# Optimization experiments

Measured on AMD Instinct MI355X. Metric: run time of the kernel, lower is better.

## Reference

```python
import jax, jax.numpy as jnp
import numpy as np

V, E, H, L, C, B, T = 50000, 1024, 512, 2, 24, 32, 512


def _lstm_layer(x, Wih, Whh, bih, bhh):
    # x: [T, B, D]; PyTorch gate order i, f, g, o stacked along 4H.
    Hh = Whh.shape[1]
    Bb = x.shape[1]
    bias = bih + bhh

    def step(carry, xt):
        h, c = carry
        g = xt @ Wih.T + h @ Whh.T + bias  # [B, 4H]
        i, f, gg, o = jnp.split(g, 4, axis=-1)
        i = jax.nn.sigmoid(i)
        f = jax.nn.sigmoid(f)
        gg = jnp.tanh(gg)
        o = jax.nn.sigmoid(o)
        c = f * c + i * gg
        h = o * jnp.tanh(c)
        return (h, c), h

    init = (jnp.zeros((Bb, Hh), x.dtype), jnp.zeros((Bb, Hh), x.dtype))
    _, hs = jax.lax.scan(step, init, x)
    return hs  # [T, B, H]


def _bilstm(x, w_ih, w_hh, b_ih, b_hh):
    # stacked weights: [L, 2(dir), 4H, D] / [L, 2, 4H, H] / [L, 2, 4H]
    out = x
    for l in range(w_ih.shape[0]):
        fwd = _lstm_layer(out, w_ih[l, 0], w_hh[l, 0], b_ih[l, 0], b_hh[l, 0])
        bwd = _lstm_layer(out[::-1], w_ih[l, 1], w_hh[l, 1], b_ih[l, 1], b_hh[l, 1])[::-1]
        out = jnp.concatenate([fwd, bwd], axis=-1)
    return out  # [T, B, 2H]


def _crf_llh(em, tags, start, end, trans):
    # em: [T, B, C], tags: [T, B]; torchcrf log-likelihood, reduction='sum', full mask.
    # numerator: score of the gold tag path
    em_sc = jnp.take_along_axis(em, tags[:, :, None], axis=2)[:, :, 0].sum(0)  # [B]
    tr_sc = trans[tags[:-1], tags[1:]].sum(0)  # [B]
    num = start[tags[0]] + em_sc + tr_sc + end[tags[-1]]

    # denominator: forward algorithm (logsumexp DP over tag dim)
    def step(alpha, em_t):
        nxt = jax.nn.logsumexp(alpha[:, :, None] + trans[None, :, :] + em_t[:, None, :], axis=1)
        return nxt, None

    alpha0 = start[None, :] + em[0]  # [B, C]
    alphaT, _ = jax.lax.scan(step, alpha0, em[1:])
    logZ = jax.nn.logsumexp(alphaT + end[None, :], axis=1)  # [B]
    return jnp.sum(num - logZ)


def setup_inputs() -> dict:
    key = jax.random.key(0)
    ks = jax.random.split(key, 12)
    k = 1.0 / np.sqrt(H)  # PyTorch LSTM/Linear init scale
    u = lambda kk, shp, s: jax.random.uniform(kk, shp, jnp.float32, -s, s)
    return {
        "x": jax.random.randint(ks[0], (B, T), 0, V),
        "labels": jax.random.randint(ks[1], (B, T), 0, C),
        "emb_table": jax.random.normal(ks[2], (V, E), jnp.float32),
        "w_ih": u(ks[3], (L, 2, 4 * H, E), k),   # E == 2H so all layers share input dim
        "w_hh": u(ks[4], (L, 2, 4 * H, H), k),
        "b_ih": u(ks[5], (L, 2, 4 * H), k),
        "b_hh": u(ks[6], (L, 2, 4 * H), k),
        "fc_w": u(ks[7], (C, 2 * H), 1.0 / np.sqrt(2 * H)),
        "fc_b": u(ks[8], (C,), 1.0 / np.sqrt(2 * H)),
        "crf_start": u(ks[9], (C,), 0.1),
        "crf_end": u(ks[10], (C,), 0.1),
        "crf_trans": u(ks[11], (C, C), 0.1),
    }


def reference(x, labels, emb_table, w_ih, w_hh, b_ih, b_hh, fc_w, fc_b, crf_start, crf_end, crf_trans):
    embed = emb_table[x]                      # [B, T, E]
    xt = jnp.transpose(embed, (1, 0, 2))      # [T, B, E]
    h = _bilstm(xt, w_ih, w_hh, b_ih, b_hh)   # [T, B, 2H] (dropout is identity in eval)
    logits = jnp.einsum('tbh,ch->tbc', h, fc_w) + fc_b  # [T, B, C]
    llh = _crf_llh(logits, jnp.transpose(labels), crf_start, crf_end, crf_trans)
    return jnp.transpose(logits, (0, 1, 2)).transpose(1, 0, 2), -llh
```

## Files before the change

### kernel.cpp

```cpp
#include <hip/hip_runtime.h>


typedef __bf16 bf16;
typedef _Float16 f16;
typedef __bf16 bf16x8 __attribute__((ext_vector_type(8)));
typedef __bf16 bf16x4 __attribute__((ext_vector_type(4)));
typedef _Float16 f16x4 __attribute__((ext_vector_type(4)));
typedef float f32x4 __attribute__((ext_vector_type(4)));
typedef unsigned int u32;
typedef unsigned long long u64;

#define TT 512
#define BB 32
#define HH 512
#define CC_ 24
#define MROWS 16384
#define KDIM 1024
#define NGATE 2048

__device__ __forceinline__ f32x4 mfma16(bf16x8 a, bf16x8 b, f32x4 c) {
  return __builtin_amdgcn_mfma_f32_16x16x32_bf16(a, b, c, 0, 0, 0);
}
__device__ __forceinline__ float sigmoidf_(float x) { return 1.f / (1.f + __expf(-x)); }
__device__ __forceinline__ float tanhf_(float x) {
  float e = __expf(2.f * x);
  return 1.f - 2.f / (e + 1.f);
}

__global__ __launch_bounds__(256) void convert_w_k(
    const float* __restrict__ wih, const float* __restrict__ whh, const float* __restrict__ fcw,
    bf16* __restrict__ wihb, bf16* __restrict__ whhb, bf16* __restrict__ fcwb) {
  const int n1 = (2 * 2 * NGATE * KDIM) / 4;
  const int n2 = (2 * 2 * NGATE * HH) / 4;
  const int n3 = (32 * KDIM) / 4;
  int stride = gridDim.x * blockDim.x;
  for (int i = blockIdx.x * blockDim.x + threadIdx.x; i < n1 + n2 + n3; i += stride) {
    float4 v;
    bf16* dst;
    if (i < n1) {
      v = ((const float4*)wih)[i];
      dst = wihb + (size_t)i * 4;
    } else if (i < n1 + n2) {
      int j = i - n1;
      v = ((const float4*)whh)[j];
      dst = whhb + (size_t)j * 4;
    } else {
      int j = i - n1 - n2;
      if ((j >> 8) < CC_) v = ((const float4*)fcw)[j];
      else                v = make_float4(0.f, 0.f, 0.f, 0.f);
      dst = fcwb + (size_t)j * 4;
    }
    bf16x4 o; o[0] = (bf16)v.x; o[1] = (bf16)v.y; o[2] = (bf16)v.z; o[3] = (bf16)v.w;
    *(bf16x4*)dst = o;
  }
}

__global__ __launch_bounds__(64) void embed_k(const int* __restrict__ x,
                                              const float* __restrict__ emb,
                                              bf16* __restrict__ xt) {
  int row = blockIdx.x;
  int t = row >> 5, b = row & 31;
  int tok = x[b * TT + t];
  const float4* src = (const float4*)(emb + (size_t)tok * KDIM);
  bf16* dst = xt + (size_t)row * KDIM;
  int i = threadIdx.x;
#pragma unroll
  for (int c = 0; c < 4; ++c) {
    float4 v = src[i + 64 * c];
    bf16x4 o; o[0] = (bf16)v.x; o[1] = (bf16)v.y; o[2] = (bf16)v.z; o[3] = (bf16)v.w;
    *(bf16x4*)(dst + (size_t)(i + 64 * c) * 4) = o;
  }
}

__global__ __launch_bounds__(256, 2) void gemm_in_k(
    const bf16* __restrict__ A, const bf16* __restrict__ W,
    const float* __restrict__ bih, const float* __restrict__ bhh,
    f16* __restrict__ Gh) {
  __shared__ bf16 As[128 * 72];
  __shared__ bf16 Ws[128 * 72];
  int dir = blockIdx.z;
  const bf16* Wd = W + (size_t)dir * NGATE * KDIM;
  const float* bi = bih + dir * NGATE;
  const float* bh = bhh + dir * NGATE;
  f16* G = Gh + (size_t)dir * 64 * MROWS * 32;
  int m0 = blockIdx.y * 128;
  int n0 = blockIdx.x * 128;
  int tid = threadIdx.x;
  int lane = tid & 63, wave = tid >> 6;
  int wm = wave >> 1, wn = wave & 1;
  int cn = lane & 15, quad = lane >> 4;

  f32x4 zz = {0.f, 0.f, 0.f, 0.f};
  f32x4 acc[4][4];
#pragma unroll
  for (int a = 0; a < 4; ++a)
#pragma unroll
    for (int b = 0; b < 4; ++b) acc[a][b] = zz;

  for (int k0 = 0; k0 < KDIM; k0 += 64) {
    __syncthreads();
#pragma unroll
    for (int j = 0; j < 4; ++j) {
      int cch = tid + 256 * j;
      int row = cch >> 3, kq = cch & 7;
      *(bf16x8*)&As[row * 72 + kq * 8] =
          *(const bf16x8*)&A[(size_t)(m0 + row) * KDIM + k0 + kq * 8];
      *(bf16x8*)&Ws[row * 72 + kq * 8] =
          *(const bf16x8*)&Wd[(size_t)(n0 + row) * KDIM + k0 + kq * 8];
    }
    __syncthreads();
#pragma unroll
    for (int kc = 0; kc < 2; ++kc) {
      bf16x8 af[4], bw[4];
#pragma unroll
      for (int mt = 0; mt < 4; ++mt)
        af[mt] = *(const bf16x8*)&As[(wm * 64 + mt * 16 + cn) * 72 + kc * 32 + quad * 8];
#pragma unroll
      for (int nt = 0; nt < 4; ++nt)
        bw[nt] = *(const bf16x8*)&Ws[(wn * 64 + nt * 16 + cn) * 72 + kc * 32 + quad * 8];
#pragma unroll
      for (int mt = 0; mt < 4; ++mt)
#pragma unroll
        for (int nt = 0; nt < 4; ++nt)
          acc[mt][nt] = mfma16(af[mt], bw[nt], acc[mt][nt]);
    }
  }
#pragma unroll
  for (int nt = 0; nt < 4; ++nt) {
    int n = n0 + wn * 64 + nt * 16 + cn;
    float bias = bi[n] + bh[n];
    int col = n & 511, gate = n >> 9;
    size_t base = (size_t)(col >> 3) * MROWS * 32 + (size_t)(col & 7) * 4 + gate;
#pragma unroll
    for (int mt = 0; mt < 4; ++mt) {
#pragma unroll
      for (int r = 0; r < 4; ++r) {
        int row = m0 + wm * 64 + mt * 16 + quad * 4 + r;
        G[base + (size_t)row * 32] = (f16)(acc[mt][nt][r] + bias);
      }
    }
  }
}

__global__ __launch_bounds__(64) void rec_k(
    const f16* __restrict__ Gin,
    const bf16* __restrict__ Whh,
    bf16* __restrict__ hbuf,
    u64* __restrict__ hx,
    u32* __restrict__ flags) {
  int wg = blockIdx.x;
  int dir = blockIdx.y;
  int lane = threadIdx.x;
  int cn = lane & 15, quad = lane >> 4;
  int j0 = wg * 8;
  const bf16* Wd = Whh + (size_t)dir * NGATE * HH;
  const f16* Gw = Gin + ((size_t)dir * 64 + wg) * MROWS * 32;
  u64* hxd = hx + (size_t)dir * TT * 4096;
  u32* fl = flags + (size_t)dir * TT * 64;

  __shared__ bf16 Bl[2 * 16 * 520];
  __shared__ bf16 hS[32][8];
  for (int c = lane; c < 2 * 16 * 64; c += 64) {
    int col = c >> 6;
    int kc8 = c & 63;
    int nt = col >> 4, ccn = col & 15;
    int gate = nt * 2 + (ccn >> 3);
    int jj_ = ccn & 7;
    int n = gate * HH + j0 + jj_;
    *(bf16x8*)&Bl[col * 520 + kc8 * 8] = *(const bf16x8*)&Wd[(size_t)n * HH + kc8 * 8];
  }
  __syncthreads();

  float cst[2][4];
#pragma unroll
  for (int mt = 0; mt < 2; ++mt)
#pragma unroll
    for (int r = 0; r < 4; ++r) cst[mt][r] = 0.f;
  bool active = cn < 8;
  int jj = cn & 7;
  f32x4 zz = {0.f, 0.f, 0.f, 0.f};

  int pb = lane >> 1, half = lane & 1;
  int sIdx = (j0 >> 5) * 256 + (((pb >= 16) ? 2 : 0) + half) * 64 +
             ((j0 >> 3) & 3) * 16 + (pb & 15);
  size_t hbOff = ((size_t)pb * KDIM + dir * HH + j0 + half * 4);

  for (int s = 0; s < TT; ++s) {
    int t = dir ? (TT - 1 - s) : s;
    f16x4 gp_[2][4];
    if (active) {
#pragma unroll
      for (int mt = 0; mt < 2; ++mt)
#pragma unroll
        for (int r = 0; r < 4; ++r) {
          int b = mt * 16 + quad * 4 + r;
          gp_[mt][r] = *(const f16x4*)&Gw[(size_t)(t * BB + b) * 32 + jj * 4];
        }
    }
    f32x4 acc[2][2];
    acc[0][0] = zz; acc[0][1] = zz; acc[1][0] = zz; acc[1][1] = zz;
    if (s > 0) {
      int tp = dir ? (t + 1) : (t - 1);
      u32* f = fl + (size_t)(s - 1) * 64;
      while (__hip_atomic_load(&f[lane], __ATOMIC_RELAXED, __HIP_MEMORY_SCOPE_AGENT) == 0u)
        __builtin_amdgcn_s_sleep(1);
      asm volatile("s_waitcnt vmcnt(0)" ::: "memory");
      const u64* hb8 = hxd + (size_t)tp * 4096;
#pragma unroll 4
      for (int kk = 0; kk < 16; ++kk) {
        union { u64 u[2]; bf16x8 v; } a0, a1;
        a0.u[0] = __hip_atomic_load(&hb8[kk * 256 + lane],       __ATOMIC_RELAXED, __HIP_MEMORY_SCOPE_AGENT);
        a0.u[1] = __hip_atomic_load(&hb8[kk * 256 + 64 + lane],  __ATOMIC_RELAXED, __HIP_MEMORY_SCOPE_AGENT);
        a1.u[0] = __hip_atomic_load(&hb8[kk * 256 + 128 + lane], __ATOMIC_RELAXED, __HIP_MEMORY_SCOPE_AGENT);
        a1.u[1] = __hip_atomic_load(&hb8[kk * 256 + 192 + lane], __ATOMIC_RELAXED, __HIP_MEMORY_SCOPE_AGENT);
        bf16x8 b0 = *(const bf16x8*)&Bl[(0 * 16 + cn) * 520 + kk * 32 + quad * 8];
        bf16x8 b1 = *(const bf16x8*)&Bl[(1 * 16 + cn) * 520 + kk * 32 + quad * 8];
        acc[0][0] = mfma16(a0.v, b0, acc[0][0]);
        acc[0][1] = mfma16(a0.v, b1, acc[0][1]);
        acc[1][0] = mfma16(a1.v, b0, acc[1][0]);
        acc[1][1] = mfma16(a1.v, b1, acc[1][1]);
      }
    }
#pragma unroll
    for (int mt = 0; mt < 2; ++mt) {
#pragma unroll
      for (int r = 0; r < 4; ++r) {
        float ip = acc[mt][0][r], gp = acc[mt][1][r];
        float fp = __shfl(ip, lane + 8);
        float op = __shfl(gp, lane + 8);
        if (active) {
          float xi = ip + (float)gp_[mt][r][0];
          float xf = fp + (float)gp_[mt][r][1];
          float xg = gp + (float)gp_[mt][r][2];
          float xo = op + (float)gp_[mt][r][3];
          float it = sigmoidf_(xi);
          float ft = sigmoidf_(xf);
          float gt = tanhf_(xg);
          float ot = sigmoidf_(xo);
          float cc = ft * cst[mt][r] + it * gt;
          cst[mt][r] = cc;
          int b = mt * 16 + quad * 4 + r;
          hS[b][jj] = (bf16)(ot * tanhf_(cc));
        }
      }
    }
    __syncthreads();
    u64 pv = *(const u64*)&hS[pb][half * 4];
    __hip_atomic_store(&hxd[(size_t)t * 4096 + sIdx], pv, __ATOMIC_RELAXED,
                       __HIP_MEMORY_SCOPE_AGENT);
    *(u64*)&hbuf[(size_t)(t * BB) * KDIM + hbOff] = pv;
    asm volatile("s_waitcnt vmcnt(0)" ::: "memory");
    if (lane == 0)
      __hip_atomic_store(&fl[(size_t)s * 64 + wg], 1u, __ATOMIC_RELAXED,
                         __HIP_MEMORY_SCOPE_AGENT);
  }
}

__global__ __launch_bounds__(64) void gemm_fc_k(
    const bf16* __restrict__ hbuf,
    const bf16* __restrict__ fcw,
    const float* __restrict__ fcb,
    float* __restrict__ outp) {
  int m0 = blockIdx.x * 16;
  int lane = threadIdx.x;
  int cn = lane & 15, quad = lane >> 4;
  f32x4 acc0 = {0.f, 0.f, 0.f, 0.f}, acc1 = {0.f, 0.f, 0.f, 0.f};
  for (int k0 = 0; k0 < KDIM; k0 += 32) {
    bf16x8 a  = *(const bf16x8*)&hbuf[(size_t)(m0 + cn) * KDIM + k0 + quad * 8];
    bf16x8 b0 = *(const bf16x8*)&fcw[(size_t)cn * KDIM + k0 + quad * 8];
    bf16x8 b1 = *(const bf16x8*)&fcw[(size_t)(cn + 16) * KDIM + k0 + quad * 8];
    acc0 = mfma16(a, b0, acc0);
    acc1 = mfma16(a, b1, acc1);
  }
#pragma unroll
  for (int r = 0; r < 4; ++r) {
    int row = m0 + quad * 4 + r;
    int t = row >> 5, b = row & 31;
    float* o = outp + (size_t)b * (TT * CC_) + (size_t)t * CC_;
    o[cn] = acc0[r] + fcb[cn];
    int c1 = cn + 16;
    if (c1 < CC_) o[c1] = acc1[r] + fcb[c1];
  }
  if (blockIdx.x == 0 && lane == 0) outp[(size_t)BB * TT * CC_] = 0.f;
}

__global__ __launch_bounds__(64) void crf_k(
    const float* __restrict__ em,
    const int* __restrict__ labels,
    const float* __restrict__ start_, const float* __restrict__ end_,
    const float* __restrict__ trans, float* __restrict__ result) {
  int b = blockIdx.x;
  int j = threadIdx.x;
  bool act = j < CC_;
  int jc = act ? j : 0;
  float tcol[CC_];
#pragma unroll
  for (int i = 0; i < CC_; ++i) tcol[i] = trans[i * CC_ + jc];
  const float* emb_ = em + (size_t)b * (TT * CC_);
  float alpha = act ? (start_[jc] + emb_[jc]) : -1e30f;
  for (int t = 1; t < TT; ++t) {
    float m = -1e30f;
#pragma unroll
    for (int i = 0; i < CC_; ++i) {
      float ai = __shfl(alpha, i);
      m = fmaxf(m, ai + tcol[i]);
    }
    float ssum = 0.f;
#pragma unroll
    for (int i = 0; i < CC_; ++i) {
      float ai = __shfl(alpha, i);
      ssum += __expf(ai + tcol[i] - m);
    }
    float na = m + __logf(ssum) + emb_[(size_t)t * CC_ + jc];
    alpha = act ? na : -1e30f;
  }
  float v = act ? (alpha + end_[jc]) : -1e30f;
  float mm = v;
#pragma unroll
  for (int off = 32; off; off >>= 1) mm = fmaxf(mm, __shfl_xor(mm, off));
  float e = act ? __expf(v - mm) : 0.f;
#pragma unroll
  for (int off = 32; off; off >>= 1) e += __shfl_xor(e, off);
  float logZ = mm + __logf(e);
  float part = 0.f;
  for (int t = j; t < TT; t += 64) {
    int tag = labels[b * TT + t];
    part += emb_[(size_t)t * CC_ + tag];
    if (t < TT - 1) part += trans[tag * CC_ + labels[b * TT + t + 1]];
  }
#pragma unroll
  for (int off = 32; off; off >>= 1) part += __shfl_xor(part, off);
  if (j == 0) {
    float num = part + start_[labels[b * TT]] + end_[labels[b * TT + TT - 1]];
    atomicAdd(result, logZ - num);
  }
}

extern "C" void kernel_launch(void* const* d_in, const int* in_sizes, int n_in,
                              void* d_out, int out_size, void* d_ws, size_t ws_size,
                              hipStream_t stream) {
  const int*   x      = (const int*)d_in[0];
  const int*   labels = (const int*)d_in[1];
  const float* emb    = (const float*)d_in[2];
  const float* w_ih   = (const float*)d_in[3];
  const float* w_hh   = (const float*)d_in[4];
  const float* b_ih   = (const float*)d_in[5];
  const float* b_hh   = (const float*)d_in[6];
  const float* fc_w   = (const float*)d_in[7];
  const float* fc_b   = (const float*)d_in[8];
  const float* crf_s  = (const float*)d_in[9];
  const float* crf_e  = (const float*)d_in[10];
  const float* crf_t  = (const float*)d_in[11];
  float* out = (float*)d_out;
  (void)in_sizes; (void)n_in; (void)out_size; (void)ws_size;

  char* ws = (char*)d_ws;
  bf16* xt    = (bf16*)ws;
  bf16* h0    = (bf16*)(ws + 33554432);
  bf16* h1    = (bf16*)(ws + 67108864);
  bf16* wihb  = (bf16*)(ws + 100663296);
  bf16* whhb  = (bf16*)(ws + 117440512);
  bf16* fcwb  = (bf16*)(ws + 125829120);
  f16*  gin   = (f16*)(ws + 125894656);
  u64*  hx    = (u64*)(ws + 260112384);
  u32*  flags = (u32*)(ws + 293666816);

  hipMemsetAsync(flags, 0, 2 * 2 * TT * 64 * sizeof(u32), stream);
  convert_w_k<<<2048, 256, 0, stream>>>(w_ih, w_hh, fc_w, wihb, whhb, fcwb);
  embed_k<<<MROWS, 64, 0, stream>>>(x, emb, xt);

  gemm_in_k<<<dim3(16, 128, 2), 256, 0, stream>>>(xt, wihb, b_ih, b_hh, gin);
  rec_k<<<dim3(64, 2), 64, 0, stream>>>(gin, whhb, h0, hx, flags);
  gemm_in_k<<<dim3(16, 128, 2), 256, 0, stream>>>(
      h0, wihb + (size_t)2 * NGATE * KDIM, b_ih + 2 * NGATE, b_hh + 2 * NGATE, gin);
  rec_k<<<dim3(64, 2), 64, 0, stream>>>(
      gin, whhb + (size_t)2 * NGATE * HH, h1, hx, flags + 2 * TT * 64);

  gemm_fc_k<<<MROWS / 16, 64, 0, stream>>>(h1, fcwb, fc_b, out);
  crf_k<<<BB, 64, 0, stream>>>(out, labels, crf_s, crf_e, crf_t,
                               out + (size_t)BB * TT * CC_);
}
```

Baseline: 9.725 ms.

## Merge both LSTM directions into one workgroup and use counter-based step sync

The recurrent kernel now has each of 64 workgroups process both the forward and backward directions, interleaved within each time step. This halves the grid and holds both directions' Whh slices in LDS. The per-workgroup flag array, which every lane polled, is replaced by one atomic counter per step that each workgroup increments and waiters poll until it reaches 64. The h exchange layout also changes so lanes read 16-byte vectors directly, and the second layer now gets separate hx and counter regions. The aim is to hide one direction's sync latency behind the other direction's work and to make polling cheaper. The cost is that the two directions are now serialized within one workgroup.

Result: slower. 13.88 ms (+42.7%).

```diff
diff --git a/kernel.cpp b/kernel.cpp
--- a/kernel.cpp
+++ b/kernel.cpp
@@ -142,117 +142,123 @@
   }
 }
 
-__global__ __launch_bounds__(64) void rec_k(
+__global__ __launch_bounds__(64) void rec2_k(
     const f16* __restrict__ Gin,
     const bf16* __restrict__ Whh,
     bf16* __restrict__ hbuf,
     u64* __restrict__ hx,
-    u32* __restrict__ flags) {
+    u32* __restrict__ cnt) {
+  __builtin_amdgcn_fence(__ATOMIC_ACQUIRE, "agent");
   int wg = blockIdx.x;
-  int dir = blockIdx.y;
   int lane = threadIdx.x;
   int cn = lane & 15, quad = lane >> 4;
   int j0 = wg * 8;
-  const bf16* Wd = Whh + (size_t)dir * NGATE * HH;
-  const f16* Gw = Gin + ((size_t)dir * 64 + wg) * MROWS * 32;
-  u64* hxd = hx + (size_t)dir * TT * 4096;
-  u32* fl = flags + (size_t)dir * TT * 64;
-
-  __shared__ bf16 Bl[2 * 16 * 520];
-  __shared__ bf16 hS[32][8];
-  for (int c = lane; c < 2 * 16 * 64; c += 64) {
-    int col = c >> 6;
-    int kc8 = c & 63;
-    int nt = col >> 4, ccn = col & 15;
-    int gate = nt * 2 + (ccn >> 3);
-    int jj_ = ccn & 7;
-    int n = gate * HH + j0 + jj_;
-    *(bf16x8*)&Bl[col * 520 + kc8 * 8] = *(const bf16x8*)&Wd[(size_t)n * HH + kc8 * 8];
+
+  __shared__ bf16 Bl[2][32 * 520];
+  __shared__ bf16 hS[2][32][8];
+
+#pragma unroll
+  for (int d = 0; d < 2; ++d) {
+    const bf16* Wd = Whh + (size_t)d * NGATE * HH;
+    for (int c = lane; c < 32 * 64; c += 64) {
+      int col = c >> 6, kc8 = c & 63;
+      int nt = col >> 4, ccn = col & 15;
+      int gate = nt * 2 + (ccn >> 3);
+      int n = gate * HH + j0 + (ccn & 7);
+      *(bf16x8*)&Bl[d][col * 520 + kc8 * 8] = *(const bf16x8*)&Wd[(size_t)n * HH + kc8 * 8];
+    }
   }
   __syncthreads();
 
-  float cst[2][4];
-#pragma unroll
-  for (int mt = 0; mt < 2; ++mt)
-#pragma unroll
-    for (int r = 0; r < 4; ++r) cst[mt][r] = 0.f;
+  float cst[2][2][4];
+#pragma unroll
+  for (int d = 0; d < 2; ++d)
+#pragma unroll
+    for (int mt = 0; mt < 2; ++mt)
+#pragma unroll
+      for (int r = 0; r < 4; ++r) cst[d][mt][r] = 0.f;
+
   bool active = cn < 8;
   int jj = cn & 7;
   f32x4 zz = {0.f, 0.f, 0.f, 0.f};
-
   int pb = lane >> 1, half = lane & 1;
-  int sIdx = (j0 >> 5) * 256 + (((pb >= 16) ? 2 : 0) + half) * 64 +
-             ((j0 >> 3) & 3) * 16 + (pb & 15);
-  size_t hbOff = ((size_t)pb * KDIM + dir * HH + j0 + half * 4);
+  const f16* Gw[2] = { Gin + (size_t)wg * MROWS * 32,
+                       Gin + (size_t)(64 + wg) * MROWS * 32 };
+  u64* hxd[2] = { hx, hx + (size_t)TT * 4096 };
 
   for (int s = 0; s < TT; ++s) {
-    int t = dir ? (TT - 1 - s) : s;
-    f16x4 gp_[2][4];
+    int tt_[2]; tt_[0] = s; tt_[1] = TT - 1 - s;
+    f16x4 gp[2][2][4];
     if (active) {
 #pragma unroll
-      for (int mt = 0; mt < 2; ++mt)
-#pragma unroll
-        for (int r = 0; r < 4; ++r) {
-          int b = mt * 16 + quad * 4 + r;
-          gp_[mt][r] = *(const f16x4*)&Gw[(size_t)(t * BB + b) * 32 + jj * 4];
-        }
-    }
-    f32x4 acc[2][2];
-    acc[0][0] = zz; acc[0][1] = zz; acc[1][0] = zz; acc[1][1] = zz;
-    if (s > 0) {
-      int tp = dir ? (t + 1) : (t - 1);
-      u32* f = fl + (size_t)(s - 1) * 64;
-      while (__hip_atomic_load(&f[lane], __ATOMIC_RELAXED, __HIP_MEMORY_SCOPE_AGENT) == 0u)
-        __builtin_amdgcn_s_sleep(1);
-      asm volatile("s_waitcnt vmcnt(0)" ::: "memory");
-      const u64* hb8 = hxd + (size_t)tp * 4096;
+      for (int d = 0; d < 2; ++d)
+#pragma unroll
+        for (int mt = 0; mt < 2; ++mt)
+#pragma unroll
+          for (int r = 0; r < 4; ++r) {
+            int b = mt * 16 + quad * 4 + r;
+            gp[d][mt][r] = *(const f16x4*)&Gw[d][(size_t)(tt_[d] * BB + b) * 32 + jj * 4];
+          }
+    }
+#pragma unroll
+    for (int d = 0; d < 2; ++d) {
+      int t = tt_[d];
+      f32x4 acc[2][2];
+      acc[0][0] = zz; acc[0][1] = zz; acc[1][0] = zz; acc[1][1] = zz;
+      if (s > 0) {
+        int tp = d ? (t + 1) : (t - 1);
+        const u32* cp = &cnt[d * TT + s - 1];
+        while (__hip_atomic_load(cp, __ATOMIC_RELAXED, __HIP_MEMORY_SCOPE_AGENT) < 64u)
+          __builtin_amdgcn_s_sleep(1);
+        asm volatile("" ::: "memory");
+        const uint4* hb16 = (const uint4*)(hxd[d] + (size_t)tp * 4096);
 #pragma unroll 4
-      for (int kk = 0; kk < 16; ++kk) {
-        union { u64 u[2]; bf16x8 v; } a0, a1;
-        a0.u[0] = __hip_atomic_load(&hb8[kk * 256 + lane],       __ATOMIC_RELAXED, __HIP_MEMORY_SCOPE_AGENT);
-        a0.u[1] = __hip_atomic_load(&hb8[kk * 256 + 64 + lane],  __ATOMIC_RELAXED, __HIP_MEMORY_SCOPE_AGENT);
-        a1.u[0] = __hip_atomic_load(&hb8[kk * 256 + 128 + lane], __ATOMIC_RELAXED, __HIP_MEMORY_SCOPE_AGENT);
-        a1.u[1] = __hip_atomic_load(&hb8[kk * 256 + 192 + lane], __ATOMIC_RELAXED, __HIP_MEMORY_SCOPE_AGENT);
-        bf16x8 b0 = *(const bf16x8*)&Bl[(0 * 16 + cn) * 520 + kk * 32 + quad * 8];
-        bf16x8 b1 = *(const bf16x8*)&Bl[(1 * 16 + cn) * 520 + kk * 32 + quad * 8];
-        acc[0][0] = mfma16(a0.v, b0, acc[0][0]);
-        acc[0][1] = mfma16(a0.v, b1, acc[0][1]);
-        acc[1][0] = mfma16(a1.v, b0, acc[1][0]);
-        acc[1][1] = mfma16(a1.v, b1, acc[1][1]);
-      }
-    }
-#pragma unroll
-    for (int mt = 0; mt < 2; ++mt) {
-#pragma unroll
-      for (int r = 0; r < 4; ++r) {
-        float ip = acc[mt][0][r], gp = acc[mt][1][r];
-        float fp = __shfl(ip, lane + 8);
-        float op = __shfl(gp, lane + 8);
-        if (active) {
-          float xi = ip + (float)gp_[mt][r][0];
-          float xf = fp + (float)gp_[mt][r][1];
-          float xg = gp + (float)gp_[mt][r][2];
-          float xo = op + (float)gp_[mt][r][3];
-          float it = sigmoidf_(xi);
-          float ft = sigmoidf_(xf);
-          float gt = tanhf_(xg);
-          float ot = sigmoidf_(xo);
-          float cc = ft * cst[mt][r] + it * gt;
-          cst[mt][r] = cc;
-          int b = mt * 16 + quad * 4 + r;
-          hS[b][jj] = (bf16)(ot * tanhf_(cc));
+        for (int kk = 0; kk < 16; ++kk) {
+          int kc = kk * 4 + quad;
+          union { uint4 u; bf16x8 v; } a0, a1;
+          a0.u = hb16[kc * 32 + cn];
+          a1.u = hb16[kc * 32 + cn + 16];
+          bf16x8 b0 = *(const bf16x8*)&Bl[d][cn * 520 + kk * 32 + quad * 8];
+          bf16x8 b1 = *(const bf16x8*)&Bl[d][(16 + cn) * 520 + kk * 32 + quad * 8];
+          acc[0][0] = mfma16(a0.v, b0, acc[0][0]);
+          acc[0][1] = mfma16(a0.v, b1, acc[0][1]);
+          acc[1][0] = mfma16(a1.v, b0, acc[1][0]);
+          acc[1][1] = mfma16(a1.v, b1, acc[1][1]);
         }
       }
-    }
-    __syncthreads();
-    u64 pv = *(const u64*)&hS[pb][half * 4];
-    __hip_atomic_store(&hxd[(size_t)t * 4096 + sIdx], pv, __ATOMIC_RELAXED,
-                       __HIP_MEMORY_SCOPE_AGENT);
-    *(u64*)&hbuf[(size_t)(t * BB) * KDIM + hbOff] = pv;
-    asm volatile("s_waitcnt vmcnt(0)" ::: "memory");
-    if (lane == 0)
-      __hip_atomic_store(&fl[(size_t)s * 64 + wg], 1u, __ATOMIC_RELAXED,
-                         __HIP_MEMORY_SCOPE_AGENT);
+#pragma unroll
+      for (int mt = 0; mt < 2; ++mt) {
+#pragma unroll
+        for (int r = 0; r < 4; ++r) {
+          float ip = acc[mt][0][r], gg = acc[mt][1][r];
+          float fp = __shfl(ip, lane + 8);
+          float op = __shfl(gg, lane + 8);
+          if (active) {
+            float xi = ip + (float)gp[d][mt][r][0];
+            float xf = fp + (float)gp[d][mt][r][1];
+            float xg = gg + (float)gp[d][mt][r][2];
+            float xo = op + (float)gp[d][mt][r][3];
+            float it = sigmoidf_(xi);
+            float ft = sigmoidf_(xf);
+            float gt = tanhf_(xg);
+            float ot = sigmoidf_(xo);
+            float cc = ft * cst[d][mt][r] + it * gt;
+            cst[d][mt][r] = cc;
+            hS[d][mt * 16 + quad * 4 + r][jj] = (bf16)(ot * tanhf_(cc));
+          }
+        }
+      }
+      __syncthreads();
+      u64 pv = *(const u64*)&hS[d][pb][half * 4];
+      __hip_atomic_store(&hxd[d][(size_t)t * 4096 + wg * 64 + lane], pv,
+                         __ATOMIC_RELAXED, __HIP_MEMORY_SCOPE_AGENT);
+      asm volatile("s_waitcnt vmcnt(0)" ::: "memory");
+      if (lane == 0)
+        __hip_atomic_fetch_add(&cnt[d * TT + s], 1u, __ATOMIC_RELAXED,
+                               __HIP_MEMORY_SCOPE_AGENT);
+      *(u64*)&hbuf[(size_t)(t * BB + pb) * KDIM + d * HH + j0 + half * 4] = pv;
+      __syncthreads();
+    }
   }
 }
 
@@ -363,18 +369,18 @@
   bf16* fcwb  = (bf16*)(ws + 125829120);
   f16*  gin   = (f16*)(ws + 125894656);
   u64*  hx    = (u64*)(ws + 260112384);
-  u32*  flags = (u32*)(ws + 293666816);
-
-  hipMemsetAsync(flags, 0, 2 * 2 * TT * 64 * sizeof(u32), stream);
+  u32*  cnt   = (u32*)(ws + 327221248);
+
+  hipMemsetAsync(cnt, 0, 2 * 2 * TT * sizeof(u32), stream);
   convert_w_k<<<2048, 256, 0, stream>>>(w_ih, w_hh, fc_w, wihb, whhb, fcwb);
   embed_k<<<MROWS, 64, 0, stream>>>(x, emb, xt);
 
   gemm_in_k<<<dim3(16, 128, 2), 256, 0, stream>>>(xt, wihb, b_ih, b_hh, gin);
-  rec_k<<<dim3(64, 2), 64, 0, stream>>>(gin, whhb, h0, hx, flags);
+  rec2_k<<<64, 64, 0, stream>>>(gin, whhb, h0, hx, cnt);
   gemm_in_k<<<dim3(16, 128, 2), 256, 0, stream>>>(
       h0, wihb + (size_t)2 * NGATE * KDIM, b_ih + 2 * NGATE, b_hh + 2 * NGATE, gin);
-  rec_k<<<dim3(64, 2), 64, 0, stream>>>(
-      gin, whhb + (size_t)2 * NGATE * HH, h1, hx, flags + 2 * TT * 64);
+  rec2_k<<<64, 64, 0, stream>>>(gin, whhb + (size_t)2 * NGATE * HH, h1,
+                                hx + (size_t)2 * TT * 4096, cnt + 2 * TT);
 
   gemm_fc_k<<<MROWS / 16, 64, 0, stream>>>(h1, fcwb, fc_b, out);
   crf_k<<<BB, 64, 0, stream>>>(out, labels, crf_s, crf_e, crf_t,
```
